# Optimization experiments

Measured on AMD Instinct MI355X. Metric: run time of the kernel, lower is better.

## Reference

```python
import jax, jax.numpy as jnp
import numpy as np

# physical / init constants (from DPINeuron.__init__ with default 1e-12 currents)
I0 = 5e-13
UT = 0.025
KAPPA = (0.75 + 0.66) / 2  # 0.705
CMEM, CAMPA, CSHUNT = 3e-12, 2e-12, 2e-12
ITAU_MEM = 1e-12
IGAIN_MEM = 1e-12
ITAU_AMPA = 1e-12
IGAIN_AMPA = 1e-12
ITH = 1e-12
IPFB_TH = 1e-12
IPFB_NORM = 1e-12
REFP = 0.0
DT = 0.001
TAU_MEM = UT / KAPPA * CMEM / ITAU_MEM
TAU_AMPA = UT / KAPPA * CAMPA / ITAU_AMPA
TAU_SHUNT = UT / KAPPA * CSHUNT / ITAU_AMPA
SLOPE = 25.0  # fast_sigmoid surrogate slope

@jax.custom_vjp
def ste_round(x):
    return jnp.round(x)

def _round_fwd(x):
    return jnp.round(x), None

def _round_bwd(_, g):
    return (g,)  # straight-through estimator

ste_round.defvjp(_round_fwd, _round_bwd)

@jax.custom_vjp
def fast_sigmoid(x):
    return (x > 0).astype(x.dtype)

def _fs_fwd(x):
    return (x > 0).astype(x.dtype), x

def _fs_bwd(x, g):
    return (g / (SLOPE * jnp.abs(x) + 1.0) ** 2,)

fast_sigmoid.defvjp(_fs_fwd, _fs_bwd)

B, N_IN, N_OUT = 4096, 2048, 2048

def setup_inputs() -> dict:
    key = jax.random.key(0)
    k1, = jax.random.split(key, 1)
    X = (jax.random.uniform(k1, (B, N_IN), dtype=jnp.float32) < 0.1).astype(jnp.float32)  # sparse input spikes
    return {
        "X": X,
        "W_ampa": jnp.ones((N_OUT, N_IN), jnp.float32),   # init.constant_(1.0)
        "W_shunt": jnp.ones((N_OUT, N_IN), jnp.float32),
        "Imem": jnp.full((B, N_OUT), I0, jnp.float32),    # initialize(): zeros + I0
        "Iampa": jnp.full((B, N_OUT), I0, jnp.float32),
        "Ishunt": jnp.full((B, N_OUT), I0, jnp.float32),
        "refractory": jnp.zeros((B, N_OUT), jnp.float32),
        "Idc": jnp.float32(1e-12),
        "Iw_ampa": jnp.float32(1e-12),
        "Iw_shunt": jnp.float32(1e-12),
        "alpha": jnp.float32(IGAIN_MEM / ITAU_MEM),       # 1.0
        "beta": jnp.float32(1.0 + I0 / ITAU_MEM),         # 1.5
    }

def reference(X, W_ampa, W_shunt, Imem, Iampa, Ishunt, refractory,
              Idc, Iw_ampa, Iw_shunt, alpha, beta):
    Iahp = I0
    Inmda = I0
    # synapse projections with STE-rounded weights: [B, n_out]
    numSynAmpa = jnp.einsum('bi,oi->bo', X, ste_round(W_ampa))
    numSynShunt = jnp.einsum('bi,oi->bo', X, ste_round(W_shunt))

    dIampa = -Iampa / TAU_AMPA
    Iampa = Iampa + (IGAIN_AMPA / ITAU_AMPA) * Iw_ampa * numSynAmpa
    dIshunt = -Ishunt / TAU_SHUNT
    Ishunt = Ishunt + (IGAIN_AMPA / ITAU_AMPA) * Iw_shunt * numSynShunt

    Iin = Idc + Iampa + Inmda - Ishunt
    Iin = Iin * (refractory <= 0)
    Iin = jnp.maximum(Iin, I0)

    Ifb = (I0 ** (1.0 / (KAPPA + 1.0))) * Imem ** (KAPPA / (KAPPA + 1.0)) \
          / (1.0 + jnp.exp(-IPFB_NORM * (Imem - IPFB_TH)))
    f_imem = Ifb / ITAU_MEM * (Imem + IGAIN_MEM)
    dImem = (alpha * (Iin - ITAU_MEM - Iahp) - beta * Imem
             + jax.lax.stop_gradient(f_imem)) / (TAU_MEM * (1.0 + IGAIN_MEM / Imem))
    Imem = jnp.maximum(Imem + dImem * DT, I0)

    # note: original code applies dIshunt decay to Iampa (kept faithful)
    Iampa = jnp.maximum(Iampa + dIampa * DT, I0)
    Iampa = jnp.maximum(Iampa + dIshunt * DT, I0)

    spike = fast_sigmoid(Imem - ITH)
    Imem = (1.0 - spike) * Imem + spike * I0
    refractory = jnp.maximum(refractory - DT, 0.0)
    refractory = (1.0 - spike) * refractory + spike * REFP
    return spike, Imem, Iampa, Ishunt, refractory
```

## Files before the change

### kernel.cpp

```cpp
#include <hip/hip_runtime.h>
#include <cmath>

#ifndef __has_builtin
#define __has_builtin(x) 0
#endif

#define B_DIM 4096
#define K_DIM 2048
#define N_DIM 2048

#define BM 128
#define BN 128
#define BK 128

typedef __attribute__((ext_vector_type(4))) float f32x4;
typedef __attribute__((ext_vector_type(4))) int i32x4;
typedef __attribute__((ext_vector_type(16))) signed char i8x16;


__device__ __forceinline__ signed char f2i8(float f) {
    int t = __float2int_rn(f);
    t = t < -127 ? -127 : (t > 127 ? 127 : t);
    return (signed char)t;
}

__device__ __forceinline__ void gl2lds16(const void* g, void* l) {
#if __has_builtin(__builtin_amdgcn_global_load_lds)
    __builtin_amdgcn_global_load_lds((__attribute__((address_space(1))) void*)g,
                                     (__attribute__((address_space(3))) void*)l,
                                     16, 0, 0);
#else
    *(uint4*)l = *(const uint4*)g;
#endif
}


__global__ void cast_x_kernel(const float* __restrict__ X,
                              signed char* __restrict__ Xb) {
    size_t i = ((size_t)blockIdx.x * 256 + threadIdx.x) * 16;
    i8x16 o;
#pragma unroll
    for (int j = 0; j < 16; j += 4) {
        f32x4 a = *(const f32x4*)(X + i + j);
        o[j]     = f2i8(a[0]);
        o[j + 1] = f2i8(a[1]);
        o[j + 2] = f2i8(a[2]);
        o[j + 3] = f2i8(a[3]);
    }
    *(i8x16*)(Xb + i) = o;
}

__global__ void cast_w_kernel(const float* __restrict__ Wa,
                              const float* __restrict__ Ws,
                              signed char* __restrict__ Wab,
                              signed char* __restrict__ Wsb) {
    size_t i = ((size_t)blockIdx.x * 256 + threadIdx.x) * 16;
    i8x16 oa, os;
#pragma unroll
    for (int j = 0; j < 16; j += 4) {
        f32x4 a = *(const f32x4*)(Wa + i + j);
        f32x4 s = *(const f32x4*)(Ws + i + j);
        oa[j]     = f2i8(a[0]); oa[j + 1] = f2i8(a[1]);
        oa[j + 2] = f2i8(a[2]); oa[j + 3] = f2i8(a[3]);
        os[j]     = f2i8(s[0]); os[j + 1] = f2i8(s[1]);
        os[j + 2] = f2i8(s[2]); os[j + 3] = f2i8(s[3]);
    }
    *(i8x16*)(Wab + i) = oa;
    *(i8x16*)(Wsb + i) = os;
}


#define RS 132

__global__ __launch_bounds__(256, 2)
void dpi_fused_kernel(const signed char* __restrict__ Xb,
                      const signed char* __restrict__ Wab,
                      const signed char* __restrict__ Wsb,
                      const float* __restrict__ gImem,
                      const float* __restrict__ gIampa,
                      const float* __restrict__ gIshunt,
                      const float* __restrict__ gRefr,
                      const float* __restrict__ pIdc,
                      const float* __restrict__ pIwa,
                      const float* __restrict__ pIws,
                      const float* __restrict__ pAlpha,
                      const float* __restrict__ pBeta,
                      float* __restrict__ out,
                      float i0pow, float kexp, float tau_mem, float inv_tau_syn)
{
    __shared__ __align__(16) unsigned char smem[49152];
    signed char* sA  = (signed char*)smem;
    signed char* sWa = (signed char*)(smem + 16384);
    signed char* sWs = (signed char*)(smem + 32768);
    float* na_buf = (float*)smem;
    float* ns_buf = (float*)(smem + 16896);

    const int tid  = threadIdx.x;
    const int lane = tid & 63;
    const int wave = tid >> 6;

    const int lin = blockIdx.x;
    const int xcd = lin & 7;
    const int loc = lin >> 3;
    const int mb  = (xcd & 3) * 8 + (loc & 7);
    const int nb  = (xcd >> 2) * 8 + (loc >> 3);
    const int m0  = mb * BM;
    const int n0  = nb * BN;

    const int wm = (wave & 1) * 64;
    const int wn = (wave >> 1) * 64;

    i32x4 accA[4][4], accS[4][4];
#pragma unroll
    for (int i = 0; i < 4; i++)
#pragma unroll
        for (int j = 0; j < 4; j++) { accA[i][j] = (i32x4)0; accS[i][j] = (i32x4)0; }

    const int frow = lane & 15;
    const int kq   = lane >> 4;
    const int swzr = frow & 7;

    for (int k0 = 0; k0 < K_DIM; k0 += BK) {
#pragma unroll
        for (int j = 0; j < 4; j++) {
            int c    = j * 256 + tid;
            int row  = c >> 3;
            int jsrc = (c & 7) ^ (row & 7);
            size_t goffA = (size_t)(m0 + row) * K_DIM + k0 + jsrc * 16;
            size_t goffW = (size_t)(n0 + row) * K_DIM + k0 + jsrc * 16;
            gl2lds16(Xb  + goffA, sA  + c * 16);
            gl2lds16(Wab + goffW, sWa + c * 16);
            gl2lds16(Wsb + goffW, sWs + c * 16);
        }
        __syncthreads();

#pragma unroll
        for (int kk = 0; kk < 2; kk++) {
            const int jb = kk * 4 + kq;
            i32x4 af[4], ba[4], bs[4];
#pragma unroll
            for (int mi = 0; mi < 4; mi++) {
                const int rA = wm + mi * 16 + frow;
                af[mi] = *(const i32x4*)(sA + rA * 128 + ((jb ^ swzr) * 16));
            }
#pragma unroll
            for (int ni = 0; ni < 4; ni++) {
                const int rB = wn + ni * 16 + frow;
                const int o  = rB * 128 + ((jb ^ swzr) * 16);
                ba[ni] = *(const i32x4*)(sWa + o);
                bs[ni] = *(const i32x4*)(sWs + o);
            }
#pragma unroll
            for (int mi = 0; mi < 4; mi++)
#pragma unroll
                for (int ni = 0; ni < 4; ni++) {
                    accA[mi][ni] = __builtin_amdgcn_mfma_i32_16x16x64_i8(af[mi], ba[ni], accA[mi][ni], 0, 0, 0);
                    accS[mi][ni] = __builtin_amdgcn_mfma_i32_16x16x64_i8(af[mi], bs[ni], accS[mi][ni], 0, 0, 0);
                }
        }
        __syncthreads();
    }

    const float idc   = *pIdc;
    const float iwa   = *pIwa;
    const float iws   = *pIws;
    const float alpha = *pAlpha;
    const float beta  = *pBeta;

    const size_t plane = (size_t)B_DIM * N_DIM;
    float* __restrict__ oSpike = out;
    float* __restrict__ oImem  = out + plane;
    float* __restrict__ oIampa = out + 2 * plane;
    float* __restrict__ oIsh   = out + 3 * plane;
    float* __restrict__ oRefr  = out + 4 * plane;

    const int rowgroup = wm >> 6;
    const int quad4    = (lane >> 4) << 2;
    const int cseg     = (tid & 31) * 4;
    const int rgrp     = tid >> 5;

#pragma unroll
    for (int s = 0; s < 4; s++) {
#pragma unroll
        for (int ni = 0; ni < 4; ni++) {
            const int lcol = wn + ni * 16 + (lane & 15);
#pragma unroll
            for (int r = 0; r < 4; r++) {
                const int lrow = rowgroup * 16 + quad4 + r;
                na_buf[lrow * RS + lcol] = (float)accA[s][ni][r];
                ns_buf[lrow * RS + lcol] = (float)accS[s][ni][r];
            }
        }
        __syncthreads();

#pragma unroll
        for (int q = 0; q < 4; q++) {
            const int lrow = rgrp * 4 + q;
            const int grow = m0 + (lrow >> 4) * 64 + s * 16 + (lrow & 15);
            const size_t idx = (size_t)grow * N_DIM + n0 + cseg;

            const f32x4 na4 = *(const f32x4*)(na_buf + lrow * RS + cseg);
            const f32x4 ns4 = *(const f32x4*)(ns_buf + lrow * RS + cseg);
            const f32x4 im4 = *(const f32x4*)(gImem   + idx);
            const f32x4 ia4 = *(const f32x4*)(gIampa  + idx);
            const f32x4 is4 = *(const f32x4*)(gIshunt + idx);
            const f32x4 rf4 = *(const f32x4*)(gRefr   + idx);

            f32x4 sp_o, im_o, ia_o, is_o, rf_o;
#pragma unroll
            for (int e = 0; e < 4; e++) {
                const float na  = na4[e];
                const float ns  = ns4[e];
                const float im  = im4[e];
                const float ia  = ia4[e];
                const float ish = is4[e];
                const float rf  = rf4[e];

                const float dIampa  = -ia * inv_tau_syn;
                const float ia2     = ia + iwa * na;
                const float dIshunt = -ish * inv_tau_syn;
                const float ish2    = ish + iws * ns;

                float Iin = idc + ia2 + 5e-13f - ish2;
                Iin = (rf <= 0.0f) ? Iin : 0.0f;
                Iin = fmaxf(Iin, 5e-13f);

                const float ifb = i0pow *
                    __builtin_amdgcn_exp2f(kexp * __builtin_amdgcn_logf(im)) * 0.5f;
                const float fimem = ifb * 1e12f * (im + 1e-12f);
                const float dImem = (alpha * ((Iin - 1e-12f) - 5e-13f) - beta * im + fimem)
                                    / (tau_mem * (1.0f + 1e-12f / im));
                float im2 = fmaxf(im + dImem * 0.001f, 5e-13f);

                float ia3 = fmaxf(ia2 + dIampa * 0.001f, 5e-13f);
                ia3       = fmaxf(ia3 + dIshunt * 0.001f, 5e-13f);

                const float spike = (im2 - 1e-12f > 0.0f) ? 1.0f : 0.0f;
                im2 = (spike > 0.0f) ? 5e-13f : im2;
                float rf2 = fmaxf(rf - 0.001f, 0.0f);
                rf2 = (spike > 0.0f) ? 0.0f : rf2;

                sp_o[e] = spike; im_o[e] = im2; ia_o[e] = ia3;
                is_o[e] = ish2;  rf_o[e] = rf2;
            }

            *(f32x4*)(oSpike + idx) = sp_o;
            *(f32x4*)(oImem  + idx) = im_o;
            *(f32x4*)(oIampa + idx) = ia_o;
            *(f32x4*)(oIsh   + idx) = is_o;
            *(f32x4*)(oRefr  + idx) = rf_o;
        }
        __syncthreads();
    }
}


extern "C" void kernel_launch(void* const* d_in, const int* in_sizes, int n_in,
                              void* d_out, int out_size, void* d_ws, size_t ws_size,
                              hipStream_t stream) {
    (void)in_sizes; (void)n_in; (void)out_size; (void)ws_size;

    const float* X       = (const float*)d_in[0];
    const float* W_ampa  = (const float*)d_in[1];
    const float* W_shunt = (const float*)d_in[2];
    const float* Imem    = (const float*)d_in[3];
    const float* Iampa   = (const float*)d_in[4];
    const float* Ishunt  = (const float*)d_in[5];
    const float* Refr    = (const float*)d_in[6];
    const float* pIdc    = (const float*)d_in[7];
    const float* pIwa    = (const float*)d_in[8];
    const float* pIws    = (const float*)d_in[9];
    const float* pAlpha  = (const float*)d_in[10];
    const float* pBeta   = (const float*)d_in[11];

    signed char* Xb  = (signed char*)d_ws;
    signed char* Wab = Xb  + (size_t)B_DIM * K_DIM;
    signed char* Wsb = Wab + (size_t)N_DIM * K_DIM;

    const float i0pow       = (float)std::pow(5e-13, 1.0 / 1.705);
    const float kexp        = (float)(0.705 / 1.705);
    const float tau_mem     = (float)(0.025 / 0.705 * 3.0);
    const float inv_tau_syn = (float)(1.0 / (0.025 / 0.705 * 2.0));

    cast_x_kernel<<<dim3((B_DIM * K_DIM) / (256 * 16)), dim3(256), 0, stream>>>(X, Xb);
    cast_w_kernel<<<dim3((N_DIM * K_DIM) / (256 * 16)), dim3(256), 0, stream>>>(
        W_ampa, W_shunt, Wab, Wsb);

    dpi_fused_kernel<<<dim3(512), dim3(256), 0, stream>>>(
        Xb, Wab, Wsb, Imem, Iampa, Ishunt, Refr,
        pIdc, pIwa, pIws, pAlpha, pBeta,
        (float*)d_out, i0pow, kexp, tau_mem, inv_tau_syn);
}
```

Measured before the change: 345.0 us.

## Double-buffer LDS tiles with BK=64 to overlap global loads with MFMA

Halves the K tile to 64 so two stages of the X, W_ampa and W_shunt tiles fit in the existing 48 KB of LDS. While the current stage is consumed by MFMAs, the next stage is prefetched asynchronously with global_load_lds. One vmcnt wait and one barrier per iteration replace the two syncthreads, and the swizzle is adapted to 64-byte rows. This hides global-load latency behind compute, at the cost of twice as many loop iterations and barriers and a new bank-conflict pattern.

Result: slower. 357.6 us (+3.7%).

```diff
diff --git a/kernel.cpp b/kernel.cpp
--- a/kernel.cpp
+++ b/kernel.cpp
@@ -11,7 +11,7 @@
 
 #define BM 128
 #define BN 128
-#define BK 128
+#define BK 64
 
 typedef __attribute__((ext_vector_type(4))) float f32x4;
 typedef __attribute__((ext_vector_type(4))) int i32x4;
@@ -34,6 +34,10 @@
 #endif
 }
 
+#define VMWAIT0   asm volatile("s_waitcnt vmcnt(0)" ::: "memory")
+#define FENCE     asm volatile("" ::: "memory")
+#define SBARRIER  do { FENCE; __builtin_amdgcn_s_barrier(); FENCE; } while (0)
+
 
 __global__ void cast_x_kernel(const float* __restrict__ X,
                               signed char* __restrict__ Xb) {
@@ -71,6 +75,31 @@
 
 
 #define RS 132
+
+__device__ __forceinline__ void stage_tile(int tt, int tid, int m0, int n0,
+                                           unsigned char* smem,
+                                           const signed char* __restrict__ Xb,
+                                           const signed char* __restrict__ Wab,
+                                           const signed char* __restrict__ Wsb) {
+    unsigned char* bb = smem + (tt & 1) * 24576;
+    const int k0s = tt * BK;
+#pragma unroll
+    for (int j = 0; j < 2; j++) {
+        const int c   = j * 256 + tid;
+        const int row = c >> 2;
+        const int js  = (c & 3) ^ ((row >> 1) & 3);
+        gl2lds16(Xb + (size_t)(m0 + row) * K_DIM + k0s + js * 16, bb + c * 16);
+    }
+#pragma unroll
+    for (int j = 0; j < 2; j++) {
+        const int c   = j * 256 + tid;
+        const int row = c >> 2;
+        const int js  = (c & 3) ^ ((row >> 1) & 3);
+        const size_t go = (size_t)(n0 + row) * K_DIM + k0s + js * 16;
+        gl2lds16(Wab + go, bb + 8192  + c * 16);
+        gl2lds16(Wsb + go, bb + 16384 + c * 16);
+    }
+}
 
 __global__ __launch_bounds__(256, 2)
 void dpi_fused_kernel(const signed char* __restrict__ Xb,
@@ -89,9 +118,6 @@
                       float i0pow, float kexp, float tau_mem, float inv_tau_syn)
 {
     __shared__ __align__(16) unsigned char smem[49152];
-    signed char* sA  = (signed char*)smem;
-    signed char* sWa = (signed char*)(smem + 16384);
-    signed char* sWs = (signed char*)(smem + 32768);
     float* na_buf = (float*)smem;
     float* ns_buf = (float*)(smem + 16896);
 
@@ -116,49 +142,43 @@
 #pragma unroll
         for (int j = 0; j < 4; j++) { accA[i][j] = (i32x4)0; accS[i][j] = (i32x4)0; }
 
-    const int frow = lane & 15;
-    const int kq   = lane >> 4;
-    const int swzr = frow & 7;
-
-    for (int k0 = 0; k0 < K_DIM; k0 += BK) {
-#pragma unroll
-        for (int j = 0; j < 4; j++) {
-            int c    = j * 256 + tid;
-            int row  = c >> 3;
-            int jsrc = (c & 7) ^ (row & 7);
-            size_t goffA = (size_t)(m0 + row) * K_DIM + k0 + jsrc * 16;
-            size_t goffW = (size_t)(n0 + row) * K_DIM + k0 + jsrc * 16;
-            gl2lds16(Xb  + goffA, sA  + c * 16);
-            gl2lds16(Wab + goffW, sWa + c * 16);
-            gl2lds16(Wsb + goffW, sWs + c * 16);
+    const int frow   = lane & 15;
+    const int kq     = lane >> 4;
+    const int slot16 = (kq ^ ((frow >> 1) & 3)) * 16;
+
+    stage_tile(0, tid, m0, n0, smem, Xb, Wab, Wsb);
+    VMWAIT0; SBARRIER;
+
+#pragma unroll 2
+    for (int t = 0; t < 32; ++t) {
+        const unsigned char* bb = smem + (t & 1) * 24576;
+        const signed char* sA  = (const signed char*)bb;
+        const signed char* sWa = (const signed char*)(bb + 8192);
+        const signed char* sWs = (const signed char*)(bb + 16384);
+
+        i32x4 af[4], ba[4], bs[4];
+#pragma unroll
+        for (int mi = 0; mi < 4; mi++)
+            af[mi] = *(const i32x4*)(sA + (wm + mi * 16 + frow) * 64 + slot16);
+#pragma unroll
+        for (int ni = 0; ni < 4; ni++) {
+            const int o = (wn + ni * 16 + frow) * 64 + slot16;
+            ba[ni] = *(const i32x4*)(sWa + o);
+            bs[ni] = *(const i32x4*)(sWs + o);
         }
-        __syncthreads();
-
-#pragma unroll
-        for (int kk = 0; kk < 2; kk++) {
-            const int jb = kk * 4 + kq;
-            i32x4 af[4], ba[4], bs[4];
-#pragma unroll
-            for (int mi = 0; mi < 4; mi++) {
-                const int rA = wm + mi * 16 + frow;
-                af[mi] = *(const i32x4*)(sA + rA * 128 + ((jb ^ swzr) * 16));
+
+        if (t < 31) stage_tile(t + 1, tid, m0, n0, smem, Xb, Wab, Wsb);
+        __builtin_amdgcn_sched_barrier(0);
+
+#pragma unroll
+        for (int mi = 0; mi < 4; mi++)
+#pragma unroll
+            for (int ni = 0; ni < 4; ni++) {
+                accA[mi][ni] = __builtin_amdgcn_mfma_i32_16x16x64_i8(af[mi], ba[ni], accA[mi][ni], 0, 0, 0);
+                accS[mi][ni] = __builtin_amdgcn_mfma_i32_16x16x64_i8(af[mi], bs[ni], accS[mi][ni], 0, 0, 0);
             }
-#pragma unroll
-            for (int ni = 0; ni < 4; ni++) {
-                const int rB = wn + ni * 16 + frow;
-                const int o  = rB * 128 + ((jb ^ swzr) * 16);
-                ba[ni] = *(const i32x4*)(sWa + o);
-                bs[ni] = *(const i32x4*)(sWs + o);
-            }
-#pragma unroll
-            for (int mi = 0; mi < 4; mi++)
-#pragma unroll
-                for (int ni = 0; ni < 4; ni++) {
-                    accA[mi][ni] = __builtin_amdgcn_mfma_i32_16x16x64_i8(af[mi], ba[ni], accA[mi][ni], 0, 0, 0);
-                    accS[mi][ni] = __builtin_amdgcn_mfma_i32_16x16x64_i8(af[mi], bs[ni], accS[mi][ni], 0, 0, 0);
-                }
-        }
-        __syncthreads();
+
+        VMWAIT0; SBARRIER;
     }
 
     const float idc   = *pIdc;
```
